# Kernel optimization log

Measured on AMD Instinct MI355X. Metric: run time of the kernel, lower is better.

The kernel has to match this reference:

```python
import jax, jax.numpy as jnp
import numpy as np

N, D, E, R, K = 8192, 1024, 8, 16, 2  # tokens, d_model, experts, lora rank, top_k


def setup_inputs() -> dict:
    key = jax.random.key(0)
    ks = jax.random.split(key, 6)
    s = 1.0 / np.sqrt(D)
    return {
        "x": jax.random.normal(ks[0], (N, D), jnp.float32),
        "W_gate": jax.random.normal(ks[1], (E, D), jnp.float32) * s,
        "A": jax.random.normal(ks[2], (E, D, R), jnp.float32) * s,
        "B": jax.random.normal(ks[3], (E, R, D), jnp.float32) * (1.0 / np.sqrt(R)),
        "W_base": jax.random.normal(ks[4], (D, D), jnp.float32) * s,
        "b_base": jax.random.normal(ks[5], (D,), jnp.float32) * 0.01,
    }


def reference(x, W_gate, A, B, W_base, b_base):
    # Gating: logits [N, E] -> top-k values/indices, softmax over the k slots
    logits = x @ W_gate.T
    topk_vals, topk_idx = jax.lax.top_k(logits, K)          # [N, K]
    w = jax.nn.softmax(topk_vals.astype(jnp.float32), axis=1).astype(x.dtype)
    # Dense combine weights [N, E]: weight for expert e if selected, else 0
    combine = jnp.sum(jax.nn.one_hot(topk_idx, E, dtype=x.dtype) * w[..., None], axis=1)
    # LoRA experts: expert_e(x) = x @ A_e @ B_e; weighted scatter-add fused via einsum
    h = jnp.einsum('nd,edr->enr', x, A)                     # [E, N, R]
    moe_out = jnp.einsum('enr,erd,ne->nd', h, B, combine)   # [N, D]
    # Base (shared) linear expert, always added when lora_experts=True
    base = x @ W_base.T + b_base
    return moe_out + base
```

## Files before the change

### kernel.cpp

```cpp
#include <hip/hip_runtime.h>
#include <stdint.h>

#define NTOK 8192
#define DM   1024
#define NE   8
#define NR   16
#define KX   1152

typedef short bf16x8 __attribute__((ext_vector_type(8)));
typedef float f32x4  __attribute__((ext_vector_type(4)));

__device__ __forceinline__ unsigned short f2bf(float f) {
    union { float f; unsigned u; } v; v.f = f;
    unsigned r = v.u + 0x7fffu + ((v.u >> 16) & 1u);
    return (unsigned short)(r >> 16);
}

__device__ __forceinline__ void gld16(const void* g, void* l) {
    __builtin_amdgcn_global_load_lds((__attribute__((address_space(1))) void*)g,
                                     (__attribute__((address_space(3))) void*)l,
                                     16, 0, 0);
}

__global__ __launch_bounds__(256) void prep(const float* __restrict__ x,
                                            const float* __restrict__ Wg,
                                            const float* __restrict__ Asrc,
                                            const float* __restrict__ Bsrc,
                                            const float* __restrict__ Wb,
                                            float* __restrict__ combine,
                                            unsigned short* __restrict__ Xext,
                                            unsigned short* __restrict__ WBext,
                                            unsigned short* __restrict__ At) {
    const int b = blockIdx.x;
    const int t = threadIdx.x;

    if (b < 2048) {
        const int lane = t & 63;
        const int w = t >> 6;
        const int n = b * 4 + w;

        const float4* x4 = (const float4*)(x + (size_t)n * DM);
        float4 xv[4];
        #pragma unroll
        for (int i = 0; i < 4; ++i) xv[i] = x4[i * 64 + lane];

        float acc[NE];
        #pragma unroll
        for (int e = 0; e < NE; ++e) {
            const float4* wg4 = (const float4*)(Wg + (size_t)e * DM);
            float s = 0.f;
            #pragma unroll
            for (int i = 0; i < 4; ++i) {
                float4 g = wg4[i * 64 + lane];
                s += xv[i].x * g.x + xv[i].y * g.y + xv[i].z * g.z + xv[i].w * g.w;
            }
            acc[e] = s;
        }
        #pragma unroll
        for (int off = 32; off >= 1; off >>= 1) {
            #pragma unroll
            for (int e = 0; e < NE; ++e) acc[e] += __shfl_xor(acc[e], off, 64);
        }
        float best = acc[0]; int bi = 0;
        #pragma unroll
        for (int e = 1; e < NE; ++e) if (acc[e] > best) { best = acc[e]; bi = e; }
        float sec = -1e30f; int si = 0;
        #pragma unroll
        for (int e = 0; e < NE; ++e) if (e != bi && acc[e] > sec) { sec = acc[e]; si = e; }
        const float ed = __expf(sec - best);
        const float w0 = 1.f / (1.f + ed);
        const float w1 = ed * w0;
        if (lane < NE)
            combine[n * NE + lane] = (lane == bi) ? w0 : ((lane == si) ? w1 : 0.f);

        unsigned short* xrow = Xext + (size_t)n * KX;
        #pragma unroll
        for (int i = 0; i < 4; ++i) {
            ushort4 o;
            o.x = f2bf(xv[i].x); o.y = f2bf(xv[i].y);
            o.z = f2bf(xv[i].z); o.w = f2bf(xv[i].w);
            *(ushort4*)(xrow + (i * 64 + lane) * 4) = o;
        }
    } else if (b < 3072) {
        const int j = b - 2048;
        unsigned short* row = WBext + (size_t)j * KX;
        float4 v = ((const float4*)(Wb + (size_t)j * DM))[t];
        ushort4 o;
        o.x = f2bf(v.x); o.y = f2bf(v.y); o.z = f2bf(v.z); o.w = f2bf(v.w);
        *(ushort4*)(row + t * 4) = o;
        if (t < 128) row[DM + t] = f2bf(Bsrc[(size_t)t * DM + j]);
    } else {
        const int p = b - 3072;
        const int e = p >> 4, r = p & 15;
        for (int d = t; d < DM; d += 256)
            At[(size_t)p * DM + d] = f2bf(Asrc[e * (DM * NR) + d * NR + r]);
    }
}

__global__ __launch_bounds__(256) void hall_kernel(unsigned short* Xext,
                                                   const unsigned short* __restrict__ At,
                                                   const float* __restrict__ combine) {
    __shared__ __align__(16) unsigned short lds[12288];
    const int t = threadIdx.x;
    const int lane = t & 63;
    const int w = t >> 6;
    const int quad = lane >> 4;
    const int l15 = lane & 15;
    const int bid = blockIdx.x;
    const int bm = bid >> 1;
    const int cb = bid & 1;
    const int n0 = bm * 32;
    const int wm = (w & 1) * 16;
    const int wn = (w >> 1) * 32;

    const int srow = t >> 3;
    const int seg  = (t & 7) ^ (srow & 7);

    const unsigned short* gX  = Xext + (size_t)(n0 + srow) * KX + seg * 8;
    const unsigned short* gA0 = At + (size_t)(cb * 64 + srow) * DM + seg * 8;
    const unsigned short* gA1 = At + (size_t)(cb * 64 + 32 + srow) * DM + seg * 8;

    f32x4 acc[2] = {};

    #define HALL_STAGE(k0, s)                                              \
        gld16(gX  + (k0), (char*)lds + (s) * 12288 + w * 1024);            \
        gld16(gA0 + (k0), (char*)lds + (s) * 12288 + 4096 + w * 1024);     \
        gld16(gA1 + (k0), (char*)lds + (s) * 12288 + 8192 + w * 1024);

    #define HALL_COMPUTE(s)                                                        \
        {                                                                          \
            const int xo = (s) * 6144, ao = (s) * 6144 + 2048;                     \
            _Pragma("unroll")                                                      \
            for (int kk = 0; kk < 2; ++kk) {                                       \
                const int gs = kk * 4 + quad;                                      \
                const int sw = (gs ^ (l15 & 7)) * 8;                               \
                bf16x8 a = *(const bf16x8*)&lds[xo + (wm + l15) * 64 + sw];        \
                _Pragma("unroll")                                                  \
                for (int jf = 0; jf < 2; ++jf) {                                   \
                    bf16x8 bb = *(const bf16x8*)&lds[ao + (wn + jf * 16 + l15) * 64 + sw]; \
                    acc[jf] = __builtin_amdgcn_mfma_f32_16x16x32_bf16(a, bb, acc[jf], 0, 0, 0); \
                }                                                                  \
            }                                                                      \
        }

    HALL_STAGE(0, 0);
    for (int k0 = 0; k0 < DM; k0 += 128) {
        __syncthreads();
        HALL_STAGE(k0 + 64, 1);
        HALL_COMPUTE(0);
        __syncthreads();
        if (k0 + 128 < DM) { HALL_STAGE(k0 + 128, 0); }
        HALL_COMPUTE(1);
    }

    #pragma unroll
    for (int jf = 0; jf < 2; ++jf) {
        const int p = cb * 64 + wn + jf * 16 + l15;
        const int e = p >> 4;
        #pragma unroll
        for (int v = 0; v < 4; ++v) {
            const int n = n0 + wm + quad * 4 + v;
            const float val = acc[jf][v] * combine[n * NE + e];
            Xext[(size_t)n * KX + DM + p] = f2bf(val);
        }
    }
    #undef HALL_STAGE
    #undef HALL_COMPUTE
}

__global__ __launch_bounds__(256, 2) void mgemm(const unsigned short* __restrict__ Xext,
                                                const unsigned short* __restrict__ WBext,
                                                const float* __restrict__ bias,
                                                float* __restrict__ out) {
    __shared__ __align__(16) unsigned short lds[32768];
    const int t = threadIdx.x;
    const int lane = t & 63;
    const int w = t >> 6;
    const int quad = lane >> 4;
    const int l15 = lane & 15;

    const int bid = blockIdx.x;
    const int xcd = bid & 7;
    const int loc = bid >> 3;
    const int bm = xcd * 8 + (loc & 7);
    const int bn = loc >> 3;

    const int wm = (w & 1) * 64;
    const int wn = (w >> 1) * 64;

    f32x4 acc[4][4] = {};

    const int srow = t >> 3;
    const int seg  = (t & 7) ^ (srow & 7);
    const unsigned short* gA = Xext  + (size_t)(bm * 128 + srow) * KX + seg * 8;
    const unsigned short* gB = WBext + (size_t)(bn * 128 + srow) * KX + seg * 8;

    #define MG_STAGE(k0, s)                                                          \
        _Pragma("unroll")                                                            \
        for (int c = 0; c < 4; ++c) {                                                \
            gld16(gA + (size_t)c * 32 * KX + (k0), (char*)lds + (s) * 32768 + c * 4096 + w * 1024);        \
            gld16(gB + (size_t)c * 32 * KX + (k0), (char*)lds + (s) * 32768 + 16384 + c * 4096 + w * 1024);\
        }

    #define MG_COMPUTE(s)                                                            \
        {                                                                            \
            const int ao = (s) * 16384, bo = (s) * 16384 + 8192;                     \
            _Pragma("unroll")                                                        \
            for (int kk = 0; kk < 2; ++kk) {                                         \
                const int gs = kk * 4 + quad;                                        \
                const int sw = (gs ^ (l15 & 7)) * 8;                                 \
                bf16x8 a[4], b[4];                                                   \
                _Pragma("unroll")                                                    \
                for (int i = 0; i < 4; ++i)                                          \
                    a[i] = *(const bf16x8*)&lds[ao + (wm + i * 16 + l15) * 64 + sw]; \
                _Pragma("unroll")                                                    \
                for (int j = 0; j < 4; ++j)                                          \
                    b[j] = *(const bf16x8*)&lds[bo + (wn + j * 16 + l15) * 64 + sw]; \
                _Pragma("unroll")                                                    \
                for (int i = 0; i < 4; ++i)                                          \
                    _Pragma("unroll")                                                \
                    for (int j = 0; j < 4; ++j)                                      \
                        acc[i][j] = __builtin_amdgcn_mfma_f32_16x16x32_bf16(a[i], b[j], acc[i][j], 0, 0, 0); \
            }                                                                        \
        }

    MG_STAGE(0, 0);
    for (int k0 = 0; k0 < KX; k0 += 128) {
        __syncthreads();
        MG_STAGE(k0 + 64, 1);
        MG_COMPUTE(0);
        __syncthreads();
        if (k0 + 128 < KX) { MG_STAGE(k0 + 128, 0); }
        MG_COMPUTE(1);
    }
    #undef MG_STAGE
    #undef MG_COMPUTE

    __syncthreads();
    float* lf = (float*)lds + w * 4096;
    #pragma unroll
    for (int j = 0; j < 4; ++j) {
        const float bv = bias[bn * 128 + wn + j * 16 + l15];
        #pragma unroll
        for (int i = 0; i < 4; ++i)
            #pragma unroll
            for (int v = 0; v < 4; ++v) {
                const int row_l = i * 16 + quad * 4 + v;
                const int col_s = (j * 16 + l15) ^ ((row_l & 1) << 4);
                lf[row_l * 64 + col_s] = acc[i][j][v] + bv;
            }
    }
    __builtin_amdgcn_s_waitcnt(0);
    #pragma unroll
    for (int rr = 0; rr < 16; ++rr) {
        const int row_r = rr * 4 + (lane >> 4);
        const int col4  = (lane & 15) * 4;
        const int col4s = col4 ^ ((row_r & 1) << 4);
        float4 vv = *(const float4*)&lf[row_r * 64 + col4s];
        *(float4*)&out[(size_t)(bm * 128 + wm + row_r) * DM + bn * 128 + wn + col4] = vv;
    }
}

extern "C" void kernel_launch(void* const* d_in, const int* in_sizes, int n_in,
                              void* d_out, int out_size, void* d_ws, size_t ws_size,
                              hipStream_t stream) {
    const float* x  = (const float*)d_in[0];
    const float* Wg = (const float*)d_in[1];
    const float* A  = (const float*)d_in[2];
    const float* B  = (const float*)d_in[3];
    const float* Wb = (const float*)d_in[4];
    const float* bb = (const float*)d_in[5];
    float* out = (float*)d_out;

    char* ws = (char*)d_ws;
    float*          combine = (float*)ws;
    unsigned short* Xext    = (unsigned short*)(ws + 262144);
    unsigned short* WBext   = (unsigned short*)(ws + 262144 + 18874368);
    unsigned short* At      = (unsigned short*)(ws + 262144 + 18874368 + 2359296);

    hipLaunchKernelGGL(prep,        dim3(3200), dim3(256), 0, stream,
                       x, Wg, A, B, Wb, combine, Xext, WBext, At);
    hipLaunchKernelGGL(hall_kernel, dim3(512),  dim3(256), 0, stream, Xext, At, combine);
    hipLaunchKernelGGL(mgemm,       dim3(512),  dim3(256), 0, stream, Xext, WBext, bb, out);
}
```

Measured before the change: 128.3 us.

## Fuse gating and bf16 conversion of x into the LoRA down-projection kernel

```diff
diff --git a/kernel.cpp b/kernel.cpp
--- a/kernel.cpp
+++ b/kernel.cpp
@@ -22,67 +22,15 @@
                                      16, 0, 0);
 }
 
-__global__ __launch_bounds__(256) void prep(const float* __restrict__ x,
-                                            const float* __restrict__ Wg,
-                                            const float* __restrict__ Asrc,
-                                            const float* __restrict__ Bsrc,
-                                            const float* __restrict__ Wb,
-                                            float* __restrict__ combine,
-                                            unsigned short* __restrict__ Xext,
-                                            unsigned short* __restrict__ WBext,
-                                            unsigned short* __restrict__ At) {
+__global__ __launch_bounds__(256) void prep2(const float* __restrict__ Bsrc,
+                                             const float* __restrict__ Wb,
+                                             const float* __restrict__ Asrc,
+                                             unsigned short* __restrict__ WBext,
+                                             unsigned short* __restrict__ At) {
     const int b = blockIdx.x;
     const int t = threadIdx.x;
-
-    if (b < 2048) {
-        const int lane = t & 63;
-        const int w = t >> 6;
-        const int n = b * 4 + w;
-
-        const float4* x4 = (const float4*)(x + (size_t)n * DM);
-        float4 xv[4];
-        #pragma unroll
-        for (int i = 0; i < 4; ++i) xv[i] = x4[i * 64 + lane];
-
-        float acc[NE];
-        #pragma unroll
-        for (int e = 0; e < NE; ++e) {
-            const float4* wg4 = (const float4*)(Wg + (size_t)e * DM);
-            float s = 0.f;
-            #pragma unroll
-            for (int i = 0; i < 4; ++i) {
-                float4 g = wg4[i * 64 + lane];
-                s += xv[i].x * g.x + xv[i].y * g.y + xv[i].z * g.z + xv[i].w * g.w;
-            }
-            acc[e] = s;
-        }
-        #pragma unroll
-        for (int off = 32; off >= 1; off >>= 1) {
-            #pragma unroll
-            for (int e = 0; e < NE; ++e) acc[e] += __shfl_xor(acc[e], off, 64);
-        }
-        float best = acc[0]; int bi = 0;
-        #pragma unroll
-        for (int e = 1; e < NE; ++e) if (acc[e] > best) { best = acc[e]; bi = e; }
-        float sec = -1e30f; int si = 0;
-        #pragma unroll
-        for (int e = 0; e < NE; ++e) if (e != bi && acc[e] > sec) { sec = acc[e]; si = e; }
-        const float ed = __expf(sec - best);
-        const float w0 = 1.f / (1.f + ed);
-        const float w1 = ed * w0;
-        if (lane < NE)
-            combine[n * NE + lane] = (lane == bi) ? w0 : ((lane == si) ? w1 : 0.f);
-
-        unsigned short* xrow = Xext + (size_t)n * KX;
-        #pragma unroll
-        for (int i = 0; i < 4; ++i) {
-            ushort4 o;
-            o.x = f2bf(xv[i].x); o.y = f2bf(xv[i].y);
-            o.z = f2bf(xv[i].z); o.w = f2bf(xv[i].w);
-            *(ushort4*)(xrow + (i * 64 + lane) * 4) = o;
-        }
-    } else if (b < 3072) {
-        const int j = b - 2048;
+    if (b < 1024) {
+        const int j = b;
         unsigned short* row = WBext + (size_t)j * KX;
         float4 v = ((const float4*)(Wb + (size_t)j * DM))[t];
         ushort4 o;
@@ -90,82 +38,122 @@
         *(ushort4*)(row + t * 4) = o;
         if (t < 128) row[DM + t] = f2bf(Bsrc[(size_t)t * DM + j]);
     } else {
-        const int p = b - 3072;
+        const int p = b - 1024;
         const int e = p >> 4, r = p & 15;
         for (int d = t; d < DM; d += 256)
             At[(size_t)p * DM + d] = f2bf(Asrc[e * (DM * NR) + d * NR + r]);
     }
 }
 
-__global__ __launch_bounds__(256) void hall_kernel(unsigned short* Xext,
-                                                   const unsigned short* __restrict__ At,
-                                                   const float* __restrict__ combine) {
-    __shared__ __align__(16) unsigned short lds[12288];
+__global__ __launch_bounds__(256) void gate_hall(const float* __restrict__ x,
+                                                 const float* __restrict__ Wg,
+                                                 const unsigned short* __restrict__ At,
+                                                 unsigned short* __restrict__ Xext) {
+    __shared__ __align__(16) unsigned short lds[18432];
     const int t = threadIdx.x;
     const int lane = t & 63;
     const int w = t >> 6;
     const int quad = lane >> 4;
     const int l15 = lane & 15;
-    const int bid = blockIdx.x;
-    const int bm = bid >> 1;
-    const int cb = bid & 1;
-    const int n0 = bm * 32;
-    const int wm = (w & 1) * 16;
-    const int wn = (w >> 1) * 32;
-
-    const int srow = t >> 3;
-    const int seg  = (t & 7) ^ (srow & 7);
-
-    const unsigned short* gX  = Xext + (size_t)(n0 + srow) * KX + seg * 8;
-    const unsigned short* gA0 = At + (size_t)(cb * 64 + srow) * DM + seg * 8;
-    const unsigned short* gA1 = At + (size_t)(cb * 64 + 32 + srow) * DM + seg * 8;
-
+    const int n0 = blockIdx.x * 16;
+
+    const int row  = t >> 4;
+    const int kseg = t & 15;
+    const int xsw  = ((kseg >> 1) ^ (row & 7)) * 8 + (kseg & 1) * 4;
+    const int brow = lane >> 3;
+    const int bseg = (lane & 7) ^ brow;
+
+    const float4* gx = (const float4*)(x + (size_t)(n0 + row) * DM);
+    unsigned short* gxb = Xext + (size_t)(n0 + row) * KX;
+
+    float gacc[NE] = {};
     f32x4 acc[2] = {};
 
-    #define HALL_STAGE(k0, s)                                              \
-        gld16(gX  + (k0), (char*)lds + (s) * 12288 + w * 1024);            \
-        gld16(gA0 + (k0), (char*)lds + (s) * 12288 + 4096 + w * 1024);     \
-        gld16(gA1 + (k0), (char*)lds + (s) * 12288 + 8192 + w * 1024);
-
-    #define HALL_COMPUTE(s)                                                        \
-        {                                                                          \
-            const int xo = (s) * 6144, ao = (s) * 6144 + 2048;                     \
-            _Pragma("unroll")                                                      \
-            for (int kk = 0; kk < 2; ++kk) {                                       \
-                const int gs = kk * 4 + quad;                                      \
-                const int sw = (gs ^ (l15 & 7)) * 8;                               \
-                bf16x8 a = *(const bf16x8*)&lds[xo + (wm + l15) * 64 + sw];        \
-                _Pragma("unroll")                                                  \
-                for (int jf = 0; jf < 2; ++jf) {                                   \
-                    bf16x8 bb = *(const bf16x8*)&lds[ao + (wn + jf * 16 + l15) * 64 + sw]; \
+    #define GH_STAGE(k0, s)                                                         \
+        {                                                                           \
+            _Pragma("unroll")                                                       \
+            for (int i = 0; i < 4; ++i) {                                           \
+                const int q = w * 4 + i;                                            \
+                gld16(At + (size_t)(q * 8 + brow) * DM + (k0) + bseg * 8,           \
+                      (char*)lds + (s) * 18432 + 2048 + q * 1024 + lane * 16);      \
+            }                                                                       \
+            float4 xv = gx[((k0) >> 2) + kseg];                                     \
+            ushort4 xo;                                                             \
+            xo.x = f2bf(xv.x); xo.y = f2bf(xv.y);                                   \
+            xo.z = f2bf(xv.z); xo.w = f2bf(xv.w);                                   \
+            *(ushort4*)&lds[(s) * 9216 + row * 64 + xsw] = xo;                      \
+            *(ushort4*)(gxb + (k0) + kseg * 4) = xo;                                \
+            _Pragma("unroll")                                                       \
+            for (int e = 0; e < NE; ++e) {                                          \
+                float4 gv = ((const float4*)(Wg + (size_t)e * DM))[((k0) >> 2) + kseg]; \
+                gacc[e] += xv.x * gv.x + xv.y * gv.y + xv.z * gv.z + xv.w * gv.w;   \
+            }                                                                       \
+        }
+
+    #define GH_COMPUTE(s)                                                           \
+        {                                                                           \
+            const int xo_ = (s) * 9216, bo_ = (s) * 9216 + 1024;                    \
+            _Pragma("unroll")                                                       \
+            for (int kk = 0; kk < 2; ++kk) {                                        \
+                const int gs = kk * 4 + quad;                                       \
+                bf16x8 a = *(const bf16x8*)&lds[xo_ + l15 * 64 + (gs ^ (l15 & 7)) * 8]; \
+                _Pragma("unroll")                                                   \
+                for (int jf = 0; jf < 2; ++jf) {                                    \
+                    const int r = (w * 2 + jf) * 16 + l15;                          \
+                    bf16x8 bb = *(const bf16x8*)&lds[bo_ + r * 64 + (gs ^ (r & 7)) * 8]; \
                     acc[jf] = __builtin_amdgcn_mfma_f32_16x16x32_bf16(a, bb, acc[jf], 0, 0, 0); \
-                }                                                                  \
-            }                                                                      \
-        }
-
-    HALL_STAGE(0, 0);
+                }                                                                   \
+            }                                                                       \
+        }
+
+    GH_STAGE(0, 0);
     for (int k0 = 0; k0 < DM; k0 += 128) {
         __syncthreads();
-        HALL_STAGE(k0 + 64, 1);
-        HALL_COMPUTE(0);
-        __syncthreads();
-        if (k0 + 128 < DM) { HALL_STAGE(k0 + 128, 0); }
-        HALL_COMPUTE(1);
-    }
+        GH_STAGE(k0 + 64, 1);
+        GH_COMPUTE(0);
+        __syncthreads();
+        if (k0 + 128 < DM) { GH_STAGE(k0 + 128, 0); }
+        GH_COMPUTE(1);
+    }
+    #undef GH_STAGE
+    #undef GH_COMPUTE
+
+    #pragma unroll
+    for (int off = 1; off <= 8; off <<= 1) {
+        #pragma unroll
+        for (int e = 0; e < NE; ++e) gacc[e] += __shfl_xor(gacc[e], off, 64);
+    }
+    float best = gacc[0]; int bi = 0;
+    #pragma unroll
+    for (int e = 1; e < NE; ++e) if (gacc[e] > best) { best = gacc[e]; bi = e; }
+    float sec = -1e30f; int si = 0;
+    #pragma unroll
+    for (int e = 0; e < NE; ++e) if (e != bi && gacc[e] > sec) { sec = gacc[e]; si = e; }
+    const float ed = __expf(sec - best);
+    const float w0 = 1.f / (1.f + ed);
+    const float w1 = ed * w0;
+
+    __syncthreads();
+    float* gsh = (float*)lds;
+    int*   ish = (int*)(gsh + 32);
+    if (kseg == 0) {
+        gsh[row] = w0; gsh[16 + row] = w1;
+        ish[row] = bi; ish[16 + row] = si;
+    }
+    __syncthreads();
 
     #pragma unroll
     for (int jf = 0; jf < 2; ++jf) {
-        const int p = cb * 64 + wn + jf * 16 + l15;
-        const int e = p >> 4;
+        const int jt = w * 2 + jf;
         #pragma unroll
         for (int v = 0; v < 4; ++v) {
-            const int n = n0 + wm + quad * 4 + v;
-            const float val = acc[jf][v] * combine[n * NE + e];
-            Xext[(size_t)n * KX + DM + p] = f2bf(val);
-        }
-    }
-    #undef HALL_STAGE
-    #undef HALL_COMPUTE
+            const int r = quad * 4 + v;
+            const float sw0 = gsh[r], sw1 = gsh[16 + r];
+            const int   sbi = ish[r], ssi = ish[16 + r];
+            const float scale = (jt == sbi) ? sw0 : ((jt == ssi) ? sw1 : 0.f);
+            Xext[(size_t)(n0 + r) * KX + DM + jt * 16 + l15] = f2bf(acc[jf][v] * scale);
+        }
+    }
 }
 
 __global__ __launch_bounds__(256, 2) void mgemm(const unsigned short* __restrict__ Xext,
@@ -273,13 +261,11 @@
     float* out = (float*)d_out;
 
     char* ws = (char*)d_ws;
-    float*          combine = (float*)ws;
-    unsigned short* Xext    = (unsigned short*)(ws + 262144);
-    unsigned short* WBext   = (unsigned short*)(ws + 262144 + 18874368);
-    unsigned short* At      = (unsigned short*)(ws + 262144 + 18874368 + 2359296);
-
-    hipLaunchKernelGGL(prep,        dim3(3200), dim3(256), 0, stream,
-                       x, Wg, A, B, Wb, combine, Xext, WBext, At);
-    hipLaunchKernelGGL(hall_kernel, dim3(512),  dim3(256), 0, stream, Xext, At, combine);
-    hipLaunchKernelGGL(mgemm,       dim3(512),  dim3(256), 0, stream, Xext, WBext, bb, out);
-}
+    unsigned short* Xext  = (unsigned short*)ws;
+    unsigned short* WBext = (unsigned short*)(ws + 18874368);
+    unsigned short* At    = (unsigned short*)(ws + 18874368 + 2359296);
+
+    hipLaunchKernelGGL(prep2,     dim3(1152), dim3(256), 0, stream, B, Wb, A, WBext, At);
+    hipLaunchKernelGGL(gate_hall, dim3(512),  dim3(256), 0, stream, x, Wg, At, Xext);
+    hipLaunchKernelGGL(mgemm,     dim3(512),  dim3(256), 0, stream, Xext, WBext, bb, out);
+}
```

Measured after the change: 141.6 us. +10.4%, slower.

## Use partial vmcnt waits and raw barriers to keep two LDS stages in flight

Applied to the files above, without the earlier changes.

```diff
diff --git a/kernel.cpp b/kernel.cpp
--- a/kernel.cpp
+++ b/kernel.cpp
@@ -21,6 +21,9 @@
                                      (__attribute__((address_space(3))) void*)l,
                                      16, 0, 0);
 }
+
+#define VM_WAIT(n) asm volatile("s_waitcnt vmcnt(" #n ")" ::: "memory")
+#define BAR() __builtin_amdgcn_s_barrier()
 
 __global__ __launch_bounds__(256) void prep(const float* __restrict__ x,
                                             const float* __restrict__ Wg,
@@ -144,13 +147,22 @@
         }
 
     HALL_STAGE(0, 0);
+    HALL_STAGE(64, 1);
     for (int k0 = 0; k0 < DM; k0 += 128) {
-        __syncthreads();
-        HALL_STAGE(k0 + 64, 1);
+        VM_WAIT(3);
+        BAR();
         HALL_COMPUTE(0);
-        __syncthreads();
-        if (k0 + 128 < DM) { HALL_STAGE(k0 + 128, 0); }
+        BAR();
+        if (k0 + 128 < DM) {
+            HALL_STAGE(k0 + 128, 0);
+            VM_WAIT(3);
+        } else {
+            VM_WAIT(0);
+        }
+        BAR();
         HALL_COMPUTE(1);
+        BAR();
+        if (k0 + 192 < DM) HALL_STAGE(k0 + 192, 1);
     }
 
     #pragma unroll
@@ -225,13 +237,22 @@
         }
 
     MG_STAGE(0, 0);
+    MG_STAGE(64, 1);
     for (int k0 = 0; k0 < KX; k0 += 128) {
-        __syncthreads();
-        MG_STAGE(k0 + 64, 1);
+        VM_WAIT(8);
+        BAR();
         MG_COMPUTE(0);
-        __syncthreads();
-        if (k0 + 128 < KX) { MG_STAGE(k0 + 128, 0); }
+        BAR();
+        if (k0 + 128 < KX) {
+            MG_STAGE(k0 + 128, 0);
+            VM_WAIT(8);
+        } else {
+            VM_WAIT(0);
+        }
+        BAR();
         MG_COMPUTE(1);
+        BAR();
+        if (k0 + 192 < KX) MG_STAGE(k0 + 192, 1);
     }
     #undef MG_STAGE
     #undef MG_COMPUTE
```

Result: no change. 129.8 us (+1.2%).

## Enlarge main GEMM tile to 256x128 with 8 waves and explicit vmcnt pipelining

Applied to the files above, without the earlier changes.

```diff
diff --git a/kernel.cpp b/kernel.cpp
--- a/kernel.cpp
+++ b/kernel.cpp
@@ -21,6 +21,9 @@
                                      (__attribute__((address_space(3))) void*)l,
                                      16, 0, 0);
 }
+
+#define VM_WAIT(n) asm volatile("s_waitcnt vmcnt(" #n ")" ::: "memory")
+#define BAR() __builtin_amdgcn_s_barrier()
 
 __global__ __launch_bounds__(256) void prep(const float* __restrict__ x,
                                             const float* __restrict__ Wg,
@@ -168,11 +171,11 @@
     #undef HALL_COMPUTE
 }
 
-__global__ __launch_bounds__(256, 2) void mgemm(const unsigned short* __restrict__ Xext,
-                                                const unsigned short* __restrict__ WBext,
-                                                const float* __restrict__ bias,
-                                                float* __restrict__ out) {
-    __shared__ __align__(16) unsigned short lds[32768];
+__global__ __launch_bounds__(512, 2) void mgemm2(const unsigned short* __restrict__ Xext,
+                                                 const unsigned short* __restrict__ WBext,
+                                                 const float* __restrict__ bias,
+                                                 float* __restrict__ out) {
+    __shared__ __align__(16) unsigned short lds[49152];
     const int t = threadIdx.x;
     const int lane = t & 63;
     const int w = t >> 6;
@@ -182,82 +185,116 @@
     const int bid = blockIdx.x;
     const int xcd = bid & 7;
     const int loc = bid >> 3;
-    const int bm = xcd * 8 + (loc & 7);
-    const int bn = loc >> 3;
-
-    const int wm = (w & 1) * 64;
-    const int wn = (w >> 1) * 64;
+    const int bm = xcd * 4 + (loc & 3);
+    const int bn = loc >> 2;
+
+    const int wm = (w & 3) * 64;
+    const int wn = (w >> 2) * 64;
 
     f32x4 acc[4][4] = {};
 
-    const int srow = t >> 3;
-    const int seg  = (t & 7) ^ (srow & 7);
-    const unsigned short* gA = Xext  + (size_t)(bm * 128 + srow) * KX + seg * 8;
-    const unsigned short* gB = WBext + (size_t)(bn * 128 + srow) * KX + seg * 8;
-
-    #define MG_STAGE(k0, s)                                                          \
-        _Pragma("unroll")                                                            \
-        for (int c = 0; c < 4; ++c) {                                                \
-            gld16(gA + (size_t)c * 32 * KX + (k0), (char*)lds + (s) * 32768 + c * 4096 + w * 1024);        \
-            gld16(gB + (size_t)c * 32 * KX + (k0), (char*)lds + (s) * 32768 + 16384 + c * 4096 + w * 1024);\
-        }
-
-    #define MG_COMPUTE(s)                                                            \
-        {                                                                            \
-            const int ao = (s) * 16384, bo = (s) * 16384 + 8192;                     \
-            _Pragma("unroll")                                                        \
-            for (int kk = 0; kk < 2; ++kk) {                                         \
-                const int gs = kk * 4 + quad;                                        \
-                const int sw = (gs ^ (l15 & 7)) * 8;                                 \
-                bf16x8 a[4], b[4];                                                   \
-                _Pragma("unroll")                                                    \
-                for (int i = 0; i < 4; ++i)                                          \
-                    a[i] = *(const bf16x8*)&lds[ao + (wm + i * 16 + l15) * 64 + sw]; \
-                _Pragma("unroll")                                                    \
-                for (int j = 0; j < 4; ++j)                                          \
-                    b[j] = *(const bf16x8*)&lds[bo + (wn + j * 16 + l15) * 64 + sw]; \
-                _Pragma("unroll")                                                    \
-                for (int i = 0; i < 4; ++i)                                          \
-                    _Pragma("unroll")                                                \
-                    for (int j = 0; j < 4; ++j)                                      \
-                        acc[i][j] = __builtin_amdgcn_mfma_f32_16x16x32_bf16(a[i], b[j], acc[i][j], 0, 0, 0); \
-            }                                                                        \
-        }
-
-    MG_STAGE(0, 0);
+    const int rbase = w * 8 + (lane >> 3);
+    const int sseg  = (lane & 7) ^ (lane >> 3);
+    const unsigned short* gA = Xext  + (size_t)(bm * 256 + rbase) * KX + sseg * 8;
+    const unsigned short* gB = WBext + (size_t)(bn * 128 + rbase) * KX + sseg * 8;
+
+    #define MG2_STAGE(k0, s)                                                        \
+        {                                                                           \
+            _Pragma("unroll")                                                       \
+            for (int i = 0; i < 4; ++i)                                             \
+                gld16(gA + (size_t)(i * 64) * KX + (k0),                            \
+                      (char*)lds + (s) * 49152 + i * 8192 + w * 1024);              \
+            _Pragma("unroll")                                                       \
+            for (int j = 0; j < 2; ++j)                                             \
+                gld16(gB + (size_t)(j * 64) * KX + (k0),                            \
+                      (char*)lds + (s) * 49152 + 32768 + j * 8192 + w * 1024);      \
+        }
+
+    bf16x8 af[2][4], bf[2][4];
+
+    #define MG2_LDFRAGS(s)                                                          \
+        {                                                                           \
+            const int ao = (s) * 24576, bo = (s) * 24576 + 16384;                   \
+            _Pragma("unroll")                                                       \
+            for (int kk = 0; kk < 2; ++kk) {                                        \
+                const int gs = kk * 4 + quad;                                       \
+                _Pragma("unroll")                                                   \
+                for (int i = 0; i < 4; ++i) {                                       \
+                    const int ra = wm + i * 16 + l15;                               \
+                    const int rb = wn + i * 16 + l15;                               \
+                    af[kk][i] = *(const bf16x8*)&lds[ao + ra * 64 + ((gs ^ (ra & 7)) * 8)]; \
+                    bf[kk][i] = *(const bf16x8*)&lds[bo + rb * 64 + ((gs ^ (rb & 7)) * 8)]; \
+                }                                                                   \
+            }                                                                       \
+        }
+
+    #define MG2_MFMA()                                                             \
+        {                                                                          \
+            _Pragma("unroll")                                                      \
+            for (int kk = 0; kk < 2; ++kk)                                         \
+                _Pragma("unroll")                                                  \
+                for (int i = 0; i < 4; ++i)                                        \
+                    _Pragma("unroll")                                              \
+                    for (int j = 0; j < 4; ++j)                                    \
+                        acc[i][j] = __builtin_amdgcn_mfma_f32_16x16x32_bf16(af[kk][i], bf[kk][j], acc[i][j], 0, 0, 0); \
+        }
+
+    MG2_STAGE(0, 0);
+    MG2_STAGE(64, 1);
     for (int k0 = 0; k0 < KX; k0 += 128) {
-        __syncthreads();
-        MG_STAGE(k0 + 64, 1);
-        MG_COMPUTE(0);
-        __syncthreads();
-        if (k0 + 128 < KX) { MG_STAGE(k0 + 128, 0); }
-        MG_COMPUTE(1);
-    }
-    #undef MG_STAGE
-    #undef MG_COMPUTE
-
-    __syncthreads();
-    float* lf = (float*)lds + w * 4096;
+        VM_WAIT(6);
+        BAR();
+        MG2_LDFRAGS(0);
+        asm volatile("s_waitcnt lgkmcnt(0)" ::: "memory");
+        __builtin_amdgcn_sched_barrier(0);
+        BAR();
+        if (k0 + 128 < KX) MG2_STAGE(k0 + 128, 0);
+        __builtin_amdgcn_s_setprio(1);
+        MG2_MFMA();
+        __builtin_amdgcn_s_setprio(0);
+        if (k0 + 128 < KX) { VM_WAIT(6); } else { VM_WAIT(0); }
+        BAR();
+        MG2_LDFRAGS(1);
+        asm volatile("s_waitcnt lgkmcnt(0)" ::: "memory");
+        __builtin_amdgcn_sched_barrier(0);
+        BAR();
+        if (k0 + 192 < KX) MG2_STAGE(k0 + 192, 1);
+        __builtin_amdgcn_s_setprio(1);
+        MG2_MFMA();
+        __builtin_amdgcn_s_setprio(0);
+    }
+    #undef MG2_STAGE
+    #undef MG2_LDFRAGS
+    #undef MG2_MFMA
+
+    BAR();
+    float* lf = (float*)lds + w * 2048;
     #pragma unroll
-    for (int j = 0; j < 4; ++j) {
-        const float bv = bias[bn * 128 + wn + j * 16 + l15];
-        #pragma unroll
-        for (int i = 0; i < 4; ++i)
+    for (int p = 0; p < 2; ++p) {
+        #pragma unroll
+        for (int j = 0; j < 4; ++j) {
+            const float bv = bias[bn * 128 + wn + j * 16 + l15];
             #pragma unroll
-            for (int v = 0; v < 4; ++v) {
-                const int row_l = i * 16 + quad * 4 + v;
-                const int col_s = (j * 16 + l15) ^ ((row_l & 1) << 4);
-                lf[row_l * 64 + col_s] = acc[i][j][v] + bv;
+            for (int ii = 0; ii < 2; ++ii) {
+                const int i = p * 2 + ii;
+                #pragma unroll
+                for (int v = 0; v < 4; ++v) {
+                    const int row_l = ii * 16 + quad * 4 + v;
+                    const int col_s = (j * 16 + l15) ^ ((row_l & 1) << 4);
+                    lf[row_l * 64 + col_s] = acc[i][j][v] + bv;
+                }
             }
-    }
-    __builtin_amdgcn_s_waitcnt(0);
-    #pragma unroll
-    for (int rr = 0; rr < 16; ++rr) {
-        const int row_r = rr * 4 + (lane >> 4);
-        const int col4  = (lane & 15) * 4;
-        const int col4s = col4 ^ ((row_r & 1) << 4);
-        float4 vv = *(const float4*)&lf[row_r * 64 + col4s];
-        *(float4*)&out[(size_t)(bm * 128 + wm + row_r) * DM + bn * 128 + wn + col4] = vv;
+        }
+        __builtin_amdgcn_s_waitcnt(0);
+        #pragma unroll
+        for (int rr = 0; rr < 8; ++rr) {
+            const int row_r = rr * 4 + (lane >> 4);
+            const int col4  = (lane & 15) * 4;
+            const int col4s = col4 ^ ((row_r & 1) << 4);
+            float4 vv = *(const float4*)&lf[row_r * 64 + col4s];
+            *(float4*)&out[(size_t)(bm * 256 + wm + p * 32 + row_r) * DM + bn * 128 + wn + col4] = vv;
+        }
+        __builtin_amdgcn_s_waitcnt(0);
     }
 }
 
@@ -281,5 +318,5 @@
     hipLaunchKernelGGL(prep,        dim3(3200), dim3(256), 0, stream,
                        x, Wg, A, B, Wb, combine, Xext, WBext, At);
     hipLaunchKernelGGL(hall_kernel, dim3(512),  dim3(256), 0, stream, Xext, At, combine);
-    hipLaunchKernelGGL(mgemm,       dim3(512),  dim3(256), 0, stream, Xext, WBext, bb, out);
-}
+    hipLaunchKernelGGL(mgemm2,      dim3(256),  dim3(512), 0, stream, Xext, WBext, bb, out);
+}
```

Measured after the change: 134.1 us. +4.6%, slower.
